# Optimization experiments

Measured on AMD Instinct MI355X. Metric: run time of the kernel, lower is better.

Reference implementation:

```python
import jax, jax.numpy as jnp
import numpy as np

N, C, T, V = 16, 256, 256, 64   # batch, node_channel_in, time, total_nodes
SC, SV = 3, 64                  # node_channel_out, num_seeds
NEW_NODES, C_OUT = 64, 3
IN_DIM = C * V + SC * SV        # 16576


def setup_inputs() -> dict:
    key = jax.random.key(0)
    k1, k2, k3, k4 = jax.random.split(key, 4)
    x = jax.random.normal(k1, (N, C, T, V), dtype=jnp.float32)
    seeds = jax.random.normal(k2, (N, T, SC, SV), dtype=jnp.float32)
    # Stacked weights of the `new_nodes` independent Linear(IN_DIM, C_OUT) layers
    W = jax.random.normal(k3, (NEW_NODES, C_OUT, IN_DIM), dtype=jnp.float32) * 0.02
    b = jax.random.normal(k4, (NEW_NODES, C_OUT), dtype=jnp.float32) * 0.02
    return {"x": x, "seeds": seeds, "W": W, "b": b}


def reference(x, seeds, W, b):
    n, c, t, v = x.shape
    # (n,c,t,v) -> (n,t,c*v)
    xm = jnp.transpose(x, (0, 2, 1, 3)).reshape(n, t, c * v)
    sm = seeds.reshape(n, t, -1)                 # (n,t,sc*sv)
    mix = jnp.concatenate([xm, sm], axis=2)      # (n,t,IN_DIM)
    # Fused horizontal GEMM over all new_nodes projections, then stacked on dim 3:
    # out[n,t,c_out,j] = sum_k mix[n,t,k] * W[j,c_out,k] + b[j,c_out]
    out = jnp.einsum('ntk,jck->ntcj', mix, W) + b.T[None, None]
    return out  # (n, t, node_channel_out, new_nodes)
```

## Files before the change

kernel.cpp:

```cpp
#include <hip/hip_runtime.h>
#include <hip/hip_bf16.h>

typedef unsigned short u16;
typedef unsigned int   u32;
typedef __attribute__((ext_vector_type(8))) short bf16x8;
typedef __attribute__((ext_vector_type(4))) float f32x4;

#define NB    16
#define CIN   256
#define TDIM  256
#define VDIM  64
#define PCOL  192
#define NCHX  256
#define NCH   259
#define MTOT  4096
#define CHUNK_U16 12288
#define WT_BYTES ((size_t)NCH * CHUNK_U16 * 2)

__device__ __forceinline__ u16 f2bf(float f) {
  u32 u = __builtin_bit_cast(u32, f);
  u32 r = u + 0x7fffu + ((u >> 16) & 1u);
  return (u16)(r >> 16);
}
__device__ __forceinline__ u32 pk2(float a, float b) {
  return (u32)f2bf(a) | ((u32)f2bf(b) << 16);
}
__device__ __forceinline__ void gload_lds16(const void* g, void* l) {
  __builtin_amdgcn_global_load_lds(
      (const __attribute__((address_space(1))) u32*)g,
      (__attribute__((address_space(3))) u32*)l, 16, 0, 0);
}

__global__ void prep_w(const float* __restrict__ W, u16* __restrict__ Wt) {
  int u  = blockIdx.x * 256 + threadIdx.x;
  int q  = u & 7;
  int p  = (u >> 3) % PCOL;
  int ch = u / (PCOL * 8);
  int j = p & 63, co = p >> 6;
  const float* src = W + (size_t)(j * 3 + co) * 16576 + ch * 64 + q * 8;
  float4 fa = *(const float4*)src;
  float4 fb = *(const float4*)(src + 4);
  uint4 v;
  v.x = pk2(fa.x, fa.y); v.y = pk2(fa.z, fa.w);
  v.z = pk2(fb.x, fb.y); v.w = pk2(fb.z, fb.w);
  ((uint4*)Wt)[(size_t)ch * 1536 + p * 8 + (q ^ (p & 7))] = v;
}

__global__ __launch_bounds__(256, 2)
void gemm_bf16(const float* __restrict__ x, const float* __restrict__ seeds,
               const u16* __restrict__ Wt, float* __restrict__ dst,
               const float* __restrict__ bias, int S) {
  __shared__ __align__(16) u16 lds[2][16384];
  const int tid  = threadIdx.x;
  const int lane = tid & 63;
  const int wid  = tid >> 6;
  const int bid  = blockIdx.x;
  int mblk, ksp;
  if (S == 8) { ksp = bid & 7;  mblk = bid >> 3; }
  else        { mblk = bid & 63; ksp = bid >> 6; }
  const int n  = mblk >> 2;
  const int t0 = (mblk & 3) << 6;
  const int c0 = (NCH * ksp) / S;
  const int c1 = (NCH * (ksp + 1)) / S;

  const int q0 = tid & 7;
  const int m0 = tid >> 3;

  f32x4 acc[4][3] = {};

  struct ASet { float4 r0a, r0b, r1a, r1b; };
  ASet AX, AY;

  auto Bi = [&](int ch, int buf) {
    const char* gsrc = (const char*)Wt + (size_t)ch * 24576 + wid * 1024 + lane * 16;
    char* lbase = (char*)&lds[buf][4096] + wid * 1024;
    #pragma unroll
    for (int r = 0; r < 6; ++r)
      gload_lds16(gsrc + (size_t)r * 4096, lbase + r * 4096);
  };
  auto Ai = [&](int ch, ASet& s) {
    const float *a0, *a1;
    if (ch < NCHX) {
      a0 = x + (((size_t)n * CIN + ch) * TDIM + (t0 + m0)) * VDIM + q0 * 8;
      a1 = a0 + (size_t)32 * VDIM;
    } else {
      a0 = seeds + ((size_t)n * TDIM + (t0 + m0)) * 192 + (ch - NCHX) * 64 + q0 * 8;
      a1 = a0 + (size_t)32 * 192;
    }
    s.r0a = *(const float4*)a0; s.r0b = *(const float4*)(a0 + 4);
    s.r1a = *(const float4*)a1; s.r1b = *(const float4*)(a1 + 4);
  };
  auto CONV = [&](const ASet& s, int buf) {
    uint4 v;
    v.x = pk2(s.r0a.x, s.r0a.y); v.y = pk2(s.r0a.z, s.r0a.w);
    v.z = pk2(s.r0b.x, s.r0b.y); v.w = pk2(s.r0b.z, s.r0b.w);
    ((uint4*)&lds[buf][0])[m0 * 8 + (q0 ^ (m0 & 7))] = v;
    int m1 = m0 + 32;
    v.x = pk2(s.r1a.x, s.r1a.y); v.y = pk2(s.r1a.z, s.r1a.w);
    v.z = pk2(s.r1b.x, s.r1b.y); v.w = pk2(s.r1b.z, s.r1b.w);
    ((uint4*)&lds[buf][0])[m1 * 8 + (q0 ^ (m1 & 7))] = v;
  };

  const int lr = lane & 15, lq = lane >> 4;
  auto COMPUTE = [&](int buf) {
    const u16* L = &lds[buf][0];
    #pragma unroll
    for (int ks = 0; ks < 2; ++ks) {
      const int q = ks * 4 + lq;
      bf16x8 af[4], bfr[3];
      #pragma unroll
      for (int mt = 0; mt < 4; ++mt) {
        int m = mt * 16 + lr;
        af[mt] = *(const bf16x8*)(L + (m * 8 + (q ^ (m & 7))) * 8);
      }
      #pragma unroll
      for (int nt = 0; nt < 3; ++nt) {
        int p = wid * 48 + nt * 16 + lr;
        bfr[nt] = *(const bf16x8*)(L + 4096 + (p * 8 + (q ^ (p & 7))) * 8);
      }
      #pragma unroll
      for (int mt = 0; mt < 4; ++mt)
        #pragma unroll
        for (int nt = 0; nt < 3; ++nt)
          acc[mt][nt] = __builtin_amdgcn_mfma_f32_16x16x32_bf16(
              af[mt], bfr[nt], acc[mt][nt], 0, 0, 0);
    }
  };

  Bi(c0, 0);
  __builtin_amdgcn_sched_barrier(0);
  Ai(c0, AX);
  if (c0 + 1 < c1) Ai(c0 + 1, AY);
  __builtin_amdgcn_sched_barrier(0);
  CONV(AX, 0);
  asm volatile("s_waitcnt lgkmcnt(0)" ::: "memory");
  __builtin_amdgcn_sched_barrier(0);
  __builtin_amdgcn_s_barrier();
  __builtin_amdgcn_sched_barrier(0);

#define PHASE(BUF, AP, AN)                                                    \
  {                                                                           \
    const bool hasN  = (ch + 1 < c1);                                         \
    const bool hasNN = (ch + 2 < c1);                                         \
    if (hasN)  Bi(ch + 1, (BUF) ^ 1);                                         \
    __builtin_amdgcn_sched_barrier(0);                                        \
    if (hasNN) Ai(ch + 2, AN);                                                \
    __builtin_amdgcn_sched_barrier(0);                                        \
    COMPUTE(BUF);                                                             \
    if (!hasN) break;                                                         \
    CONV(AP, (BUF) ^ 1);                                                      \
    if (hasNN) { asm volatile("s_waitcnt vmcnt(4)" ::: "memory"); }           \
    else       { asm volatile("s_waitcnt vmcnt(0)" ::: "memory"); }           \
    asm volatile("s_waitcnt lgkmcnt(0)" ::: "memory");                        \
    __builtin_amdgcn_sched_barrier(0);                                        \
    __builtin_amdgcn_s_barrier();                                             \
    __builtin_amdgcn_sched_barrier(0);                                        \
  }

  int ch = c0;
  while (true) {
    PHASE(0, AY, AX)
    ++ch;
    PHASE(1, AX, AY)
    ++ch;
  }
#undef PHASE

  float* dbase = dst + (size_t)ksp * MTOT * PCOL;
  #pragma unroll
  for (int mt = 0; mt < 4; ++mt)
    #pragma unroll
    for (int nt = 0; nt < 3; ++nt) {
      int col = wid * 48 + nt * 16 + lr;
      float bv = bias ? bias[(col & 63) * 3 + (col >> 6)] : 0.f;
      #pragma unroll
      for (int r = 0; r < 4; ++r) {
        int row = mblk * 64 + mt * 16 + lq * 4 + r;
        dbase[(size_t)row * PCOL + col] = acc[mt][nt][r] + bv;
      }
    }
}

__global__ void reduce_k(const float* __restrict__ part, const float* __restrict__ b,
                         float* __restrict__ out, int S) {
  int i4 = (blockIdx.x * 256 + threadIdx.x) * 4;
  float4 a = *(const float4*)&part[i4];
  for (int s = 1; s < S; ++s) {
    const float4 v = *(const float4*)&part[(size_t)s * (MTOT * PCOL) + i4];
    a.x += v.x; a.y += v.y; a.z += v.z; a.w += v.w;
  }
  int p0 = i4 % PCOL;
  a.x += b[((p0 + 0) & 63) * 3 + ((p0 + 0) >> 6)];
  a.y += b[((p0 + 1) & 63) * 3 + ((p0 + 1) >> 6)];
  a.z += b[((p0 + 2) & 63) * 3 + ((p0 + 2) >> 6)];
  a.w += b[((p0 + 3) & 63) * 3 + ((p0 + 3) >> 6)];
  *(float4*)&out[i4] = a;
}

__global__ void fallback_k(const float* __restrict__ x, const float* __restrict__ seeds,
                           const float* __restrict__ W, const float* __restrict__ b,
                           float* __restrict__ out) {
  __shared__ float mk[512];
  int m = blockIdx.x, n = m >> 8, t = m & 255, p = threadIdx.x;
  float acc = 0.f;
  for (int k0 = 0; k0 < 16576; k0 += 512) {
    int kn = min(512, 16576 - k0);
    __syncthreads();
    for (int i = threadIdx.x; i < kn; i += 256) {
      int k = k0 + i;
      mk[i] = (k < 16384)
                ? x[(((size_t)n * 256 + (k >> 6)) * 256 + t) * 64 + (k & 63)]
                : seeds[((size_t)n * 256 + t) * 192 + (k - 16384)];
    }
    __syncthreads();
    if (p < PCOL) {
      const float* wr = W + (size_t)((p & 63) * 3 + (p >> 6)) * 16576 + k0;
      for (int i = 0; i < kn; ++i) acc += mk[i] * wr[i];
    }
  }
  if (p < PCOL) out[(size_t)m * PCOL + p] = acc + b[(p & 63) * 3 + (p >> 6)];
}

extern "C" void kernel_launch(void* const* d_in, const int* in_sizes, int n_in,
                              void* d_out, int out_size, void* d_ws, size_t ws_size,
                              hipStream_t stream) {
  (void)in_sizes; (void)n_in; (void)out_size;
  const float* x     = (const float*)d_in[0];
  const float* seeds = (const float*)d_in[1];
  const float* W     = (const float*)d_in[2];
  const float* b     = (const float*)d_in[3];
  float* out = (float*)d_out;

  if (ws_size < WT_BYTES) {
    fallback_k<<<dim3(MTOT), dim3(256), 0, stream>>>(x, seeds, W, b, out);
    return;
  }
  u16* Wt = (u16*)d_ws;
  int S = 8;
  while (S > 1 && WT_BYTES + (size_t)S * MTOT * PCOL * 4 > ws_size) S >>= 1;
  if (WT_BYTES + (size_t)S * MTOT * PCOL * 4 > ws_size) S = 1;

  prep_w<<<dim3((NCH * PCOL * 8) / 256), dim3(256), 0, stream>>>(W, Wt);
  if (S == 1) {
    gemm_bf16<<<dim3(64), dim3(256), 0, stream>>>(x, seeds, Wt, out, b, 1);
  } else {
    float* part = (float*)((char*)d_ws + WT_BYTES);
    gemm_bf16<<<dim3(64 * S), dim3(256), 0, stream>>>(x, seeds, Wt, part, nullptr, S);
    reduce_k<<<dim3(MTOT * PCOL / 4 / 256), dim3(256), 0, stream>>>(part, b, out, S);
  }
}
```

Baseline: 81.40 us.

## Load weight B-fragments directly into registers instead of staging through LDS

```diff
diff --git a/kernel.cpp b/kernel.cpp
--- a/kernel.cpp
+++ b/kernel.cpp
@@ -24,11 +24,6 @@
 }
 __device__ __forceinline__ u32 pk2(float a, float b) {
   return (u32)f2bf(a) | ((u32)f2bf(b) << 16);
-}
-__device__ __forceinline__ void gload_lds16(const void* g, void* l) {
-  __builtin_amdgcn_global_load_lds(
-      (const __attribute__((address_space(1))) u32*)g,
-      (__attribute__((address_space(3))) u32*)l, 16, 0, 0);
 }
 
 __global__ void prep_w(const float* __restrict__ W, u16* __restrict__ Wt) {
@@ -43,14 +38,14 @@
   uint4 v;
   v.x = pk2(fa.x, fa.y); v.y = pk2(fa.z, fa.w);
   v.z = pk2(fb.x, fb.y); v.w = pk2(fb.z, fb.w);
-  ((uint4*)Wt)[(size_t)ch * 1536 + p * 8 + (q ^ (p & 7))] = v;
+  ((uint4*)Wt)[(size_t)ch * 1536 + p * 8 + q] = v;
 }
 
 __global__ __launch_bounds__(256, 2)
 void gemm_bf16(const float* __restrict__ x, const float* __restrict__ seeds,
                const u16* __restrict__ Wt, float* __restrict__ dst,
                const float* __restrict__ bias, int S) {
-  __shared__ __align__(16) u16 lds[2][16384];
+  __shared__ __align__(16) u16 ldsA[2][4096];
   const int tid  = threadIdx.x;
   const int lane = tid & 63;
   const int wid  = tid >> 6;
@@ -65,19 +60,17 @@
 
   const int q0 = tid & 7;
   const int m0 = tid >> 3;
+  const int lr = lane & 15, lq = lane >> 4;
 
   f32x4 acc[4][3] = {};
 
   struct ASet { float4 r0a, r0b, r1a, r1b; };
+  struct BSet { uint4 k0n0, k0n1, k0n2, k1n0, k1n1, k1n2; };
   ASet AX, AY;
-
-  auto Bi = [&](int ch, int buf) {
-    const char* gsrc = (const char*)Wt + (size_t)ch * 24576 + wid * 1024 + lane * 16;
-    char* lbase = (char*)&lds[buf][4096] + wid * 1024;
-    #pragma unroll
-    for (int r = 0; r < 6; ++r)
-      gload_lds16(gsrc + (size_t)r * 4096, lbase + r * 4096);
-  };
+  BSet BX, BY;
+
+  const char* bgran = (const char*)Wt + ((wid * 48 + lr) * 8 + lq) * 16;
+
   auto Ai = [&](int ch, ASet& s) {
     const float *a0, *a1;
     if (ch < NCHX) {
@@ -90,45 +83,48 @@
     s.r0a = *(const float4*)a0; s.r0b = *(const float4*)(a0 + 4);
     s.r1a = *(const float4*)a1; s.r1b = *(const float4*)(a1 + 4);
   };
+  auto Bi = [&](int ch, BSet& s) {
+    const uint4* g = (const uint4*)(bgran + (size_t)ch * 24576);
+    s.k0n0 = g[0];   s.k1n0 = g[4];
+    s.k0n1 = g[128]; s.k1n1 = g[132];
+    s.k0n2 = g[256]; s.k1n2 = g[260];
+  };
   auto CONV = [&](const ASet& s, int buf) {
     uint4 v;
     v.x = pk2(s.r0a.x, s.r0a.y); v.y = pk2(s.r0a.z, s.r0a.w);
     v.z = pk2(s.r0b.x, s.r0b.y); v.w = pk2(s.r0b.z, s.r0b.w);
-    ((uint4*)&lds[buf][0])[m0 * 8 + (q0 ^ (m0 & 7))] = v;
+    ((uint4*)&ldsA[buf][0])[m0 * 8 + (q0 ^ (m0 & 7))] = v;
     int m1 = m0 + 32;
     v.x = pk2(s.r1a.x, s.r1a.y); v.y = pk2(s.r1a.z, s.r1a.w);
     v.z = pk2(s.r1b.x, s.r1b.y); v.w = pk2(s.r1b.z, s.r1b.w);
-    ((uint4*)&lds[buf][0])[m1 * 8 + (q0 ^ (m1 & 7))] = v;
-  };
-
-  const int lr = lane & 15, lq = lane >> 4;
-  auto COMPUTE = [&](int buf) {
-    const u16* L = &lds[buf][0];
+    ((uint4*)&ldsA[buf][0])[m1 * 8 + (q0 ^ (m1 & 7))] = v;
+  };
+
+  auto COMPUTE = [&](int buf, const BSet& B) {
+    const u16* L = &ldsA[buf][0];
     #pragma unroll
     for (int ks = 0; ks < 2; ++ks) {
       const int q = ks * 4 + lq;
-      bf16x8 af[4], bfr[3];
+      bf16x8 af[4];
       #pragma unroll
       for (int mt = 0; mt < 4; ++mt) {
         int m = mt * 16 + lr;
         af[mt] = *(const bf16x8*)(L + (m * 8 + (q ^ (m & 7))) * 8);
       }
+      bf16x8 b0 = __builtin_bit_cast(bf16x8, ks ? B.k1n0 : B.k0n0);
+      bf16x8 b1 = __builtin_bit_cast(bf16x8, ks ? B.k1n1 : B.k0n1);
+      bf16x8 b2 = __builtin_bit_cast(bf16x8, ks ? B.k1n2 : B.k0n2);
       #pragma unroll
-      for (int nt = 0; nt < 3; ++nt) {
-        int p = wid * 48 + nt * 16 + lr;
-        bfr[nt] = *(const bf16x8*)(L + 4096 + (p * 8 + (q ^ (p & 7))) * 8);
+      for (int mt = 0; mt < 4; ++mt) {
+        acc[mt][0] = __builtin_amdgcn_mfma_f32_16x16x32_bf16(af[mt], b0, acc[mt][0], 0, 0, 0);
+        acc[mt][1] = __builtin_amdgcn_mfma_f32_16x16x32_bf16(af[mt], b1, acc[mt][1], 0, 0, 0);
+        acc[mt][2] = __builtin_amdgcn_mfma_f32_16x16x32_bf16(af[mt], b2, acc[mt][2], 0, 0, 0);
       }
-      #pragma unroll
-      for (int mt = 0; mt < 4; ++mt)
-        #pragma unroll
-        for (int nt = 0; nt < 3; ++nt)
-          acc[mt][nt] = __builtin_amdgcn_mfma_f32_16x16x32_bf16(
-              af[mt], bfr[nt], acc[mt][nt], 0, 0, 0);
-    }
-  };
-
-  Bi(c0, 0);
-  __builtin_amdgcn_sched_barrier(0);
+    }
+  };
+
+  Bi(c0, BX);
+  if (c0 + 1 < c1) Bi(c0 + 1, BY);
   Ai(c0, AX);
   if (c0 + 1 < c1) Ai(c0 + 1, AY);
   __builtin_amdgcn_sched_barrier(0);
@@ -138,19 +134,17 @@
   __builtin_amdgcn_s_barrier();
   __builtin_amdgcn_sched_barrier(0);
 
-#define PHASE(BUF, AP, AN)                                                    \
+#define PHASE(BUF, AP, AN, BC)                                                \
   {                                                                           \
     const bool hasN  = (ch + 1 < c1);                                         \
     const bool hasNN = (ch + 2 < c1);                                         \
-    if (hasN)  Bi(ch + 1, (BUF) ^ 1);                                         \
-    __builtin_amdgcn_sched_barrier(0);                                        \
     if (hasNN) Ai(ch + 2, AN);                                                \
     __builtin_amdgcn_sched_barrier(0);                                        \
-    COMPUTE(BUF);                                                             \
+    COMPUTE(BUF, BC);                                                         \
+    __builtin_amdgcn_sched_barrier(0);                                        \
+    if (hasNN) Bi(ch + 2, BC);                  \
     if (!hasN) break;                                                         \
     CONV(AP, (BUF) ^ 1);                                                      \
-    if (hasNN) { asm volatile("s_waitcnt vmcnt(4)" ::: "memory"); }           \
-    else       { asm volatile("s_waitcnt vmcnt(0)" ::: "memory"); }           \
     asm volatile("s_waitcnt lgkmcnt(0)" ::: "memory");                        \
     __builtin_amdgcn_sched_barrier(0);                                        \
     __builtin_amdgcn_s_barrier();                                             \
@@ -159,9 +153,9 @@
 
   int ch = c0;
   while (true) {
-    PHASE(0, AY, AX)
+    PHASE(0, AY, AX, BX)
     ++ch;
-    PHASE(1, AX, AY)
+    PHASE(1, AX, AY, BY)
     ++ch;
   }
 #undef PHASE
```

Result: slower. 91.31 us (+12.2%).
